# Kernel tuning notes

Hardware: AMD Instinct MI355X
Metric: run time of the kernel (lower is better)

## Reference

```python
import jax, jax.numpy as jnp
import numpy as np

H = 256
V_IN = 32000
V_OUT = 32000
T = 2048


def setup_inputs() -> dict:
    key = jax.random.key(0)
    ks = jax.random.split(key, 16)
    s = 1.0 / np.sqrt(H)
    inp = {
        "src": jax.random.randint(ks[0], (T, 1), 0, V_IN, dtype=jnp.int64 if jax.config.jax_enable_x64 else jnp.int32),
        "trg": jax.random.randint(ks[1], (T, 1), 0, V_OUT, dtype=jnp.int64 if jax.config.jax_enable_x64 else jnp.int32),
        "enc_emb": jax.random.normal(ks[2], (V_IN, H), jnp.float32),
        "enc_W_ih": jax.random.uniform(ks[3], (3 * H, H), jnp.float32, -s, s),
        "enc_W_hh": jax.random.uniform(ks[4], (3 * H, H), jnp.float32, -s, s),
        "enc_b_ih": jax.random.uniform(ks[5], (3 * H,), jnp.float32, -s, s),
        "enc_b_hh": jax.random.uniform(ks[6], (3 * H,), jnp.float32, -s, s),
        "dec_emb": jax.random.normal(ks[7], (V_OUT, H), jnp.float32),
        "dec_W_ih": jax.random.uniform(ks[8], (3 * H, H), jnp.float32, -s, s),
        "dec_W_hh": jax.random.uniform(ks[9], (3 * H, H), jnp.float32, -s, s),
        "dec_b_ih": jax.random.uniform(ks[10], (3 * H,), jnp.float32, -s, s),
        "dec_b_hh": jax.random.uniform(ks[11], (3 * H,), jnp.float32, -s, s),
        "out_W": jax.random.uniform(ks[12], (V_OUT, H), jnp.float32, -s, s),
        "out_b": jax.random.uniform(ks[13], (V_OUT,), jnp.float32, -s, s),
    }
    return inp


def _gru_step(x, h, W_ih, W_hh, b_ih, b_hh):
    # PyTorch GRU cell math. x,h: [H]
    gi = W_ih @ x + b_ih          # [3H]
    gh = W_hh @ h + b_hh          # [3H]
    i_r, i_z, i_n = jnp.split(gi, 3)
    h_r, h_z, h_n = jnp.split(gh, 3)
    r = jax.nn.sigmoid(i_r + h_r)
    z = jax.nn.sigmoid(i_z + h_z)
    n = jnp.tanh(i_n + r * h_n)
    return (1.0 - z) * n + z * h


def reference(src, trg, enc_emb, enc_W_ih, enc_W_hh, enc_b_ih, enc_b_hh,
              dec_emb, dec_W_ih, dec_W_hh, dec_b_ih, dec_b_hh, out_W, out_b):
    src_t = src[:, 0]  # [T], batch forced to 1 by .view(1,1,-1)
    trg_t = trg[:, 0]  # [T]
    h0 = jnp.zeros((H,), enc_emb.dtype)

    def step(h, toks):
        s_tok, t_tok = toks
        # encoder step
        h = _gru_step(enc_emb[s_tok], h, enc_W_ih, enc_W_hh, enc_b_ih, enc_b_hh)
        # decoder step (relu on embedding per source)
        x_d = jax.nn.relu(dec_emb[t_tok])
        h = _gru_step(x_d, h, dec_W_ih, dec_W_hh, dec_b_ih, dec_b_hh)
        logits = out_W @ h + out_b          # [V_OUT]
        return h, jax.nn.log_softmax(logits)

    _, outs = jax.lax.scan(step, h0, (src_t, trg_t))
    return outs[:, None, :]  # [T, 1, V_OUT]
```

## Files before the change

### kernel.cpp

```cpp
#include <hip/hip_runtime.h>
#include <hip/hip_bf16.h>

#define T_STEPS 2048
#define HDIM 256
#define VOUT 32000

#if defined(__has_builtin)
#if __has_builtin(__builtin_amdgcn_sdot4)
#define HAVE_SDOT4 1
#endif
#endif

__device__ __forceinline__ int dot4i8(int a, int b, int c) {
#ifdef HAVE_SDOT4
    return __builtin_amdgcn_sdot4(a, b, c, false);
#else
#pragma unroll
    for (int k = 0; k < 4; ++k) {
        int av = (a << (24 - 8 * k)) >> 24;
        int bv = (b << (24 - 8 * k)) >> 24;
        c += av * bv;
    }
    return c;
#endif
}

__device__ __forceinline__ float fast_sigmoid(float x) {
    return 1.0f / (1.0f + __expf(-x));
}
__device__ __forceinline__ float fast_tanh(float x) {
    float ax = fabsf(x);
    float e = __expf(-2.0f * ax);
    float t = 1.0f - 2.0f * e / (1.0f + e);
    return copysignf(t, x);
}

__global__ void k_quant(const float* __restrict__ W, int* __restrict__ wq,
                        float* __restrict__ sc) {
    int row = blockIdx.x;
    int t = threadIdx.x;
    float4 w = ((const float4*)(W + (size_t)row * HDIM))[t];
    float m = fmaxf(fmaxf(fabsf(w.x), fabsf(w.y)), fmaxf(fabsf(w.z), fabsf(w.w)));
#pragma unroll
    for (int off = 32; off; off >>= 1) m = fmaxf(m, __shfl_xor(m, off));
    float inv = (m > 0.0f) ? 127.0f / m : 0.0f;
    float scale = (m > 0.0f) ? m * (1.0f / 127.0f) : 0.0f;
    int q0 = __float2int_rn(w.x * inv); q0 = max(-127, min(127, q0));
    int q1 = __float2int_rn(w.y * inv); q1 = max(-127, min(127, q1));
    int q2 = __float2int_rn(w.z * inv); q2 = max(-127, min(127, q2));
    int q3 = __float2int_rn(w.w * inv); q3 = max(-127, min(127, q3));
    int packed = (q0 & 255) | ((q1 & 255) << 8) | ((q2 & 255) << 16) | ((q3 & 255) << 24);
    wq[row * 64 + t] = packed;
    if (t == 0) sc[row] = scale;
}

__global__ __launch_bounds__(256) void k_gi(const int* __restrict__ toks,
                                            const float* __restrict__ emb,
                                            const float* __restrict__ W,
                                            const float* __restrict__ b,
                                            float* __restrict__ gi, int do_relu) {
    __shared__ float4 xs[64];
    int t = blockIdx.x;
    int tid = threadIdx.x;
    int tok = toks[t];
    if (tid < 64) {
        float4 x = ((const float4*)(emb + (size_t)tok * HDIM))[tid];
        if (do_relu) {
            x.x = fmaxf(x.x, 0.0f); x.y = fmaxf(x.y, 0.0f);
            x.z = fmaxf(x.z, 0.0f); x.w = fmaxf(x.w, 0.0f);
        }
        xs[tid] = x;
    }
    __syncthreads();
#pragma unroll
    for (int g = 0; g < 3; ++g) {
        int row = tid + g * 256;
        const float4* wr = (const float4*)(W + (size_t)row * HDIM);
        float acc = b[row];
#pragma unroll 16
        for (int k = 0; k < 64; ++k) {
            float4 w = wr[k];
            float4 x = xs[k];
            acc += w.x * x.x + w.y * x.y + w.z * x.z + w.w * x.w;
        }
        gi[(size_t)t * 768 + row] = acc;
    }
}

__global__ __launch_bounds__(768, 3) void k_gru(
    const int* __restrict__ wq_e, const float* __restrict__ sc_e,
    const float* __restrict__ bhh_e, const float* __restrict__ gi_e,
    const int* __restrict__ wq_d, const float* __restrict__ sc_d,
    const float* __restrict__ bhh_d, const float* __restrict__ gi_d,
    float* __restrict__ h_all) {
    __shared__ float Y[768];
    __shared__ float GN[256];
    __shared__ __align__(16) int HQ[64];

    const int tid = threadIdx.x;
    const int row = tid;

    int we[64], wd[64];
    {
        const int4* pe = (const int4*)(wq_e + row * 64);
        const int4* pd = (const int4*)(wq_d + row * 64);
#pragma unroll
        for (int i = 0; i < 16; ++i) {
            int4 a = pe[i];
            int4 bq = pd[i];
            we[4 * i + 0] = a.x;  we[4 * i + 1] = a.y;
            we[4 * i + 2] = a.z;  we[4 * i + 3] = a.w;
            wd[4 * i + 0] = bq.x; wd[4 * i + 1] = bq.y;
            wd[4 * i + 2] = bq.z; wd[4 * i + 3] = bq.w;
        }
    }
    const float se = sc_e[row] * (1.0f / 127.0f);
    const float sd = sc_d[row] * (1.0f / 127.0f);
    const float be = bhh_e[row];
    const float bd = bhh_d[row];
    const bool lead = (tid < 256);
    float h = 0.0f;
    if (tid < 64) HQ[tid] = 0;
    __syncthreads();

    const float* ge = gi_e + row;
    const float* gd = gi_d + row;
    float* hop = h_all + tid;

    for (int t = 0; t < T_STEPS; ++t) {
        float gie = *ge; ge += 768;
        float gid = *gd; gd += 768;

        {
            int acc = 0;
            const int4* hq4 = (const int4*)HQ;
#pragma unroll
            for (int c = 0; c < 16; ++c) {
                int4 hv = hq4[c];
                acc = dot4i8(we[4 * c + 0], hv.x, acc);
                acc = dot4i8(we[4 * c + 1], hv.y, acc);
                acc = dot4i8(we[4 * c + 2], hv.z, acc);
                acc = dot4i8(we[4 * c + 3], hv.w, acc);
            }
            float y = se * (float)acc + be;
            if (row < 512) Y[row] = y + gie;
            else { Y[row] = y; GN[row - 512] = gie; }
        }
        __syncthreads();
        if (lead) {
            float r = fast_sigmoid(Y[tid]);
            float z = fast_sigmoid(Y[256 + tid]);
            float n = fast_tanh(GN[tid] + r * Y[512 + tid]);
            h = (1.0f - z) * n + z * h;
            ((signed char*)HQ)[tid] = (signed char)__float2int_rn(h * 127.0f);
        }
        __syncthreads();

        {
            int acc = 0;
            const int4* hq4 = (const int4*)HQ;
#pragma unroll
            for (int c = 0; c < 16; ++c) {
                int4 hv = hq4[c];
                acc = dot4i8(wd[4 * c + 0], hv.x, acc);
                acc = dot4i8(wd[4 * c + 1], hv.y, acc);
                acc = dot4i8(wd[4 * c + 2], hv.z, acc);
                acc = dot4i8(wd[4 * c + 3], hv.w, acc);
            }
            float y = sd * (float)acc + bd;
            if (row < 512) Y[row] = y + gid;
            else { Y[row] = y; GN[row - 512] = gid; }
        }
        __syncthreads();
        if (lead) {
            float r = fast_sigmoid(Y[tid]);
            float z = fast_sigmoid(Y[256 + tid]);
            float n = fast_tanh(GN[tid] + r * Y[512 + tid]);
            h = (1.0f - z) * n + z * h;
            *hop = h; hop += 256;
            ((signed char*)HQ)[tid] = (signed char)__float2int_rn(h * 127.0f);
        }
        __syncthreads();
    }
}

__global__ __launch_bounds__(256) void k_logits(const float* __restrict__ h_all,
                                                const float* __restrict__ out_W,
                                                const float* __restrict__ out_b,
                                                float* __restrict__ out) {
    __shared__ float As[64][68];
    __shared__ float Bs[64][68];
    const int vb = blockIdx.x * 64;
    const int tb = blockIdx.y * 64;
    const int tid = threadIdx.x;
    const int tx = tid & 15;
    const int ty = tid >> 4;
    const int tl = tid & 63;
    const int kg = tid >> 6;

    float acc[4][4];
#pragma unroll
    for (int i = 0; i < 4; ++i)
#pragma unroll
        for (int j = 0; j < 4; ++j) acc[i][j] = 0.0f;

    for (int k0 = 0; k0 < HDIM; k0 += 64) {
#pragma unroll
        for (int j = 0; j < 4; ++j) {
            float4 a = *(const float4*)&h_all[(size_t)(tb + tl) * HDIM + k0 + kg * 16 + 4 * j];
            int kk = kg * 16 + 4 * j;
            As[kk + 0][tl] = a.x; As[kk + 1][tl] = a.y;
            As[kk + 2][tl] = a.z; As[kk + 3][tl] = a.w;
            float4 b = *(const float4*)&out_W[(size_t)(vb + tl) * HDIM + k0 + kg * 16 + 4 * j];
            Bs[kk + 0][tl] = b.x; Bs[kk + 1][tl] = b.y;
            Bs[kk + 2][tl] = b.z; Bs[kk + 3][tl] = b.w;
        }
        __syncthreads();
#pragma unroll 16
        for (int k = 0; k < 64; ++k) {
            float4 a = *(const float4*)&As[k][ty * 4];
            float4 b = *(const float4*)&Bs[k][tx * 4];
            acc[0][0] += a.x * b.x; acc[0][1] += a.x * b.y; acc[0][2] += a.x * b.z; acc[0][3] += a.x * b.w;
            acc[1][0] += a.y * b.x; acc[1][1] += a.y * b.y; acc[1][2] += a.y * b.z; acc[1][3] += a.y * b.w;
            acc[2][0] += a.z * b.x; acc[2][1] += a.z * b.y; acc[2][2] += a.z * b.z; acc[2][3] += a.z * b.w;
            acc[3][0] += a.w * b.x; acc[3][1] += a.w * b.y; acc[3][2] += a.w * b.z; acc[3][3] += a.w * b.w;
        }
        __syncthreads();
    }
    float4 bias = *(const float4*)&out_b[vb + tx * 4];
#pragma unroll
    for (int i = 0; i < 4; ++i) {
        float4 o;
        o.x = acc[i][0] + bias.x; o.y = acc[i][1] + bias.y;
        o.z = acc[i][2] + bias.z; o.w = acc[i][3] + bias.w;
        *(float4*)&out[(size_t)(tb + ty * 4 + i) * VOUT + vb + tx * 4] = o;
    }
}

__global__ __launch_bounds__(256) void k_lse(const float* __restrict__ out,
                                             float* __restrict__ lse) {
    const int t = blockIdx.x;
    const int tid = threadIdx.x;
    const float* rowp = out + (size_t)t * VOUT;
    float m = -3.0e38f, l = 0.0f;
    for (int v = tid; v < VOUT; v += 256) {
        float x = rowp[v];
        float M = fmaxf(m, x);
        l = l * __expf(m - M) + __expf(x - M);
        m = M;
    }
#pragma unroll
    for (int off = 32; off; off >>= 1) {
        float m2 = __shfl_xor(m, off);
        float l2 = __shfl_xor(l, off);
        float M = fmaxf(m, m2);
        l = l * __expf(m - M) + l2 * __expf(m2 - M);
        m = M;
    }
    __shared__ float sm[4], sl[4];
    int lane = tid & 63, w = tid >> 6;
    if (lane == 0) { sm[w] = m; sl[w] = l; }
    __syncthreads();
    if (tid == 0) {
        float M = fmaxf(fmaxf(sm[0], sm[1]), fmaxf(sm[2], sm[3]));
        float L = sl[0] * __expf(sm[0] - M) + sl[1] * __expf(sm[1] - M) +
                  sl[2] * __expf(sm[2] - M) + sl[3] * __expf(sm[3] - M);
        lse[t] = M + __logf(L);
    }
}

__global__ __launch_bounds__(256) void k_sub(float* __restrict__ out,
                                             const float* __restrict__ lse) {
    const int t = blockIdx.y;
    const int v4 = blockIdx.x * 256 + threadIdx.x;
    if (v4 < VOUT / 4) {
        float s = lse[t];
        float4* p = (float4*)(out + (size_t)t * VOUT) + v4;
        float4 o = *p;
        o.x -= s; o.y -= s; o.z -= s; o.w -= s;
        *p = o;
    }
}

extern "C" void kernel_launch(void* const* d_in, const int* in_sizes, int n_in,
                              void* d_out, int out_size, void* d_ws, size_t ws_size,
                              hipStream_t stream) {
    (void)in_sizes; (void)n_in; (void)out_size; (void)ws_size;
    const int*   src      = (const int*)d_in[0];
    const int*   trg      = (const int*)d_in[1];
    const float* enc_emb  = (const float*)d_in[2];
    const float* enc_W_ih = (const float*)d_in[3];
    const float* enc_W_hh = (const float*)d_in[4];
    const float* enc_b_ih = (const float*)d_in[5];
    const float* enc_b_hh = (const float*)d_in[6];
    const float* dec_emb  = (const float*)d_in[7];
    const float* dec_W_ih = (const float*)d_in[8];
    const float* dec_W_hh = (const float*)d_in[9];
    const float* dec_b_ih = (const float*)d_in[10];
    const float* dec_b_hh = (const float*)d_in[11];
    const float* out_W    = (const float*)d_in[12];
    const float* out_b    = (const float*)d_in[13];
    float* out = (float*)d_out;

    char* ws = (char*)d_ws;
    float* gi_e  = (float*)ws; ws += (size_t)T_STEPS * 768 * 4;
    float* gi_d  = (float*)ws; ws += (size_t)T_STEPS * 768 * 4;
    float* h_all = (float*)ws; ws += (size_t)T_STEPS * HDIM * 4;
    float* lse   = (float*)ws; ws += (size_t)T_STEPS * 4;
    float* sc_e  = (float*)ws; ws += 768 * 4;
    float* sc_d  = (float*)ws; ws += 768 * 4;
    int*   wq_e  = (int*)ws;   ws += 768 * 64 * 4;
    int*   wq_d  = (int*)ws;   ws += 768 * 64 * 4;

    k_quant<<<768, 64, 0, stream>>>(enc_W_hh, wq_e, sc_e);
    k_quant<<<768, 64, 0, stream>>>(dec_W_hh, wq_d, sc_d);
    k_gi<<<T_STEPS, 256, 0, stream>>>(src, enc_emb, enc_W_ih, enc_b_ih, gi_e, 0);
    k_gi<<<T_STEPS, 256, 0, stream>>>(trg, dec_emb, dec_W_ih, dec_b_ih, gi_d, 1);
    k_gru<<<1, 768, 0, stream>>>(wq_e, sc_e, enc_b_hh, gi_e,
                                 wq_d, sc_d, dec_b_hh, gi_d, h_all);
    k_logits<<<dim3(VOUT / 64, T_STEPS / 64), 256, 0, stream>>>(h_all, out_W, out_b, out);
    k_lse<<<T_STEPS, 256, 0, stream>>>(out, lse);
    k_sub<<<dim3(32, T_STEPS), 256, 0, stream>>>(out, lse);
}
```

Baseline: 4.596 ms.

## Use bf16 MFMA for logits GEMM and split GRU row dot products across lanes

The output projection GEMM now runs on bf16 MFMA 16x16x32 instructions instead of an fp32 LDS-tiled FMA loop, with new conversion kernels that turn out_W and h_all into bf16. Separately, the GRU recurrent matvec is reorganised so each lane handles a quarter of the K dimension for four rows, combined with xor shuffles. This shortens the serial dot-product chain on the per-step critical path. Converting to bf16 lowers logits precision, and the extra conversion passes add memory traffic.

Result: faster. 4.463 ms (-2.9%).

```diff
diff --git a/kernel.cpp b/kernel.cpp
--- a/kernel.cpp
+++ b/kernel.cpp
@@ -4,6 +4,9 @@
 #define T_STEPS 2048
 #define HDIM 256
 #define VOUT 32000
+
+typedef short short8 __attribute__((ext_vector_type(8)));
+typedef float f32x4 __attribute__((ext_vector_type(4)));
 
 #if defined(__has_builtin)
 #if __has_builtin(__builtin_amdgcn_sdot4)
@@ -52,6 +55,22 @@
     int packed = (q0 & 255) | ((q1 & 255) << 8) | ((q2 & 255) << 16) | ((q3 & 255) << 24);
     wq[row * 64 + t] = packed;
     if (t == 0) sc[row] = scale;
+}
+
+__global__ __launch_bounds__(256) void k_cvt(const float* __restrict__ in,
+                                             unsigned short* __restrict__ out, int n4) {
+    int i = blockIdx.x * 256 + threadIdx.x;
+    if (i < n4) {
+        float4 v = ((const float4*)in)[i];
+        unsigned int u[4] = {__float_as_uint(v.x), __float_as_uint(v.y),
+                             __float_as_uint(v.z), __float_as_uint(v.w)};
+        ushort4 o;
+        o.x = (unsigned short)((u[0] + 0x7FFFu + ((u[0] >> 16) & 1)) >> 16);
+        o.y = (unsigned short)((u[1] + 0x7FFFu + ((u[1] >> 16) & 1)) >> 16);
+        o.z = (unsigned short)((u[2] + 0x7FFFu + ((u[2] >> 16) & 1)) >> 16);
+        o.w = (unsigned short)((u[3] + 0x7FFFu + ((u[3] >> 16) & 1)) >> 16);
+        ((ushort4*)out)[i] = o;
+    }
 }
 
 __global__ __launch_bounds__(256) void k_gi(const int* __restrict__ toks,
@@ -98,53 +117,74 @@
     __shared__ __align__(16) int HQ[64];
 
     const int tid = threadIdx.x;
-    const int row = tid;
-
-    int we[64], wd[64];
-    {
-        const int4* pe = (const int4*)(wq_e + row * 64);
-        const int4* pd = (const int4*)(wq_d + row * 64);
-#pragma unroll
-        for (int i = 0; i < 16; ++i) {
+    const int w = tid >> 6;
+    const int l = tid & 63;
+    const int c = l & 3;
+    const int g = l >> 2;
+
+    int we[4][16], wd[4][16];
+#pragma unroll
+    for (int j = 0; j < 4; ++j) {
+        const int4* pe = (const int4*)(wq_e + ((w * 64 + g * 4 + j) * 64 + c * 16));
+        const int4* pd = (const int4*)(wq_d + ((w * 64 + g * 4 + j) * 64 + c * 16));
+#pragma unroll
+        for (int i = 0; i < 4; ++i) {
             int4 a = pe[i];
+            we[j][4 * i + 0] = a.x; we[j][4 * i + 1] = a.y;
+            we[j][4 * i + 2] = a.z; we[j][4 * i + 3] = a.w;
             int4 bq = pd[i];
-            we[4 * i + 0] = a.x;  we[4 * i + 1] = a.y;
-            we[4 * i + 2] = a.z;  we[4 * i + 3] = a.w;
-            wd[4 * i + 0] = bq.x; wd[4 * i + 1] = bq.y;
-            wd[4 * i + 2] = bq.z; wd[4 * i + 3] = bq.w;
-        }
-    }
-    const float se = sc_e[row] * (1.0f / 127.0f);
-    const float sd = sc_d[row] * (1.0f / 127.0f);
-    const float be = bhh_e[row];
-    const float bd = bhh_d[row];
+            wd[j][4 * i + 0] = bq.x; wd[j][4 * i + 1] = bq.y;
+            wd[j][4 * i + 2] = bq.z; wd[j][4 * i + 3] = bq.w;
+        }
+    }
+    const float se = sc_e[tid] * (1.0f / 127.0f);
+    const float sd = sc_d[tid] * (1.0f / 127.0f);
+    const float be = bhh_e[tid];
+    const float bd = bhh_d[tid];
     const bool lead = (tid < 256);
+    const int c0 = c & 1;
+    const int c1 = c & 2;
     float h = 0.0f;
     if (tid < 64) HQ[tid] = 0;
     __syncthreads();
 
-    const float* ge = gi_e + row;
-    const float* gd = gi_d + row;
+    const float* ge = gi_e + tid;
+    const float* gd = gi_d + tid;
     float* hop = h_all + tid;
+    const int4* hq4 = (const int4*)HQ;
 
     for (int t = 0; t < T_STEPS; ++t) {
         float gie = *ge; ge += 768;
         float gid = *gd; gd += 768;
 
         {
-            int acc = 0;
-            const int4* hq4 = (const int4*)HQ;
-#pragma unroll
-            for (int c = 0; c < 16; ++c) {
-                int4 hv = hq4[c];
-                acc = dot4i8(we[4 * c + 0], hv.x, acc);
-                acc = dot4i8(we[4 * c + 1], hv.y, acc);
-                acc = dot4i8(we[4 * c + 2], hv.z, acc);
-                acc = dot4i8(we[4 * c + 3], hv.w, acc);
+            int4 h0 = hq4[c * 4 + 0];
+            int4 h1 = hq4[c * 4 + 1];
+            int4 h2 = hq4[c * 4 + 2];
+            int4 h3 = hq4[c * 4 + 3];
+            int p[4];
+#pragma unroll
+            for (int j = 0; j < 4; ++j) {
+                int a = 0;
+                a = dot4i8(we[j][0], h0.x, a);  a = dot4i8(we[j][1], h0.y, a);
+                a = dot4i8(we[j][2], h0.z, a);  a = dot4i8(we[j][3], h0.w, a);
+                a = dot4i8(we[j][4], h1.x, a);  a = dot4i8(we[j][5], h1.y, a);
+                a = dot4i8(we[j][6], h1.z, a);  a = dot4i8(we[j][7], h1.w, a);
+                a = dot4i8(we[j][8], h2.x, a);  a = dot4i8(we[j][9], h2.y, a);
+                a = dot4i8(we[j][10], h2.z, a); a = dot4i8(we[j][11], h2.w, a);
+                a = dot4i8(we[j][12], h3.x, a); a = dot4i8(we[j][13], h3.y, a);
+                a = dot4i8(we[j][14], h3.z, a); a = dot4i8(we[j][15], h3.w, a);
+                p[j] = a;
             }
-            float y = se * (float)acc + be;
-            if (row < 512) Y[row] = y + gie;
-            else { Y[row] = y; GN[row - 512] = gie; }
+            int s0 = c0 ? p[0] : p[1];
+            int s1 = c0 ? p[2] : p[3];
+            int r0 = (c0 ? p[1] : p[0]) + __shfl_xor(s0, 1);
+            int r1 = (c0 ? p[3] : p[2]) + __shfl_xor(s1, 1);
+            int s2 = c1 ? r0 : r1;
+            int fin = (c1 ? r1 : r0) + __shfl_xor(s2, 2);
+            float y = se * (float)fin + be;
+            if (tid < 512) Y[tid] = y + gie;
+            else { Y[tid] = y; GN[tid - 512] = gie; }
         }
         __syncthreads();
         if (lead) {
@@ -157,19 +197,33 @@
         __syncthreads();
 
         {
-            int acc = 0;
-            const int4* hq4 = (const int4*)HQ;
-#pragma unroll
-            for (int c = 0; c < 16; ++c) {
-                int4 hv = hq4[c];
-                acc = dot4i8(wd[4 * c + 0], hv.x, acc);
-                acc = dot4i8(wd[4 * c + 1], hv.y, acc);
-                acc = dot4i8(wd[4 * c + 2], hv.z, acc);
-                acc = dot4i8(wd[4 * c + 3], hv.w, acc);
+            int4 h0 = hq4[c * 4 + 0];
+            int4 h1 = hq4[c * 4 + 1];
+            int4 h2 = hq4[c * 4 + 2];
+            int4 h3 = hq4[c * 4 + 3];
+            int p[4];
+#pragma unroll
+            for (int j = 0; j < 4; ++j) {
+                int a = 0;
+                a = dot4i8(wd[j][0], h0.x, a);  a = dot4i8(wd[j][1], h0.y, a);
+                a = dot4i8(wd[j][2], h0.z, a);  a = dot4i8(wd[j][3], h0.w, a);
+                a = dot4i8(wd[j][4], h1.x, a);  a = dot4i8(wd[j][5], h1.y, a);
+                a = dot4i8(wd[j][6], h1.z, a);  a = dot4i8(wd[j][7], h1.w, a);
+                a = dot4i8(wd[j][8], h2.x, a);  a = dot4i8(wd[j][9], h2.y, a);
+                a = dot4i8(wd[j][10], h2.z, a); a = dot4i8(wd[j][11], h2.w, a);
+                a = dot4i8(wd[j][12], h3.x, a); a = dot4i8(wd[j][13], h3.y, a);
+                a = dot4i8(wd[j][14], h3.z, a); a = dot4i8(wd[j][15], h3.w, a);
+                p[j] = a;
             }
-            float y = sd * (float)acc + bd;
-            if (row < 512) Y[row] = y + gid;
-            else { Y[row] = y; GN[row - 512] = gid; }
+            int s0 = c0 ? p[0] : p[1];
+            int s1 = c0 ? p[2] : p[3];
+            int r0 = (c0 ? p[1] : p[0]) + __shfl_xor(s0, 1);
+            int r1 = (c0 ? p[3] : p[2]) + __shfl_xor(s1, 1);
+            int s2 = c1 ? r0 : r1;
+            int fin = (c1 ? r1 : r0) + __shfl_xor(s2, 2);
+            float y = sd * (float)fin + bd;
+            if (tid < 512) Y[tid] = y + gid;
+            else { Y[tid] = y; GN[tid - 512] = gid; }
         }
         __syncthreads();
         if (lead) {
@@ -184,56 +238,47 @@
     }
 }
 
-__global__ __launch_bounds__(256) void k_logits(const float* __restrict__ h_all,
-                                                const float* __restrict__ out_W,
+__global__ __launch_bounds__(256) void k_logits(const unsigned short* __restrict__ hb,
+                                                const unsigned short* __restrict__ wb,
                                                 const float* __restrict__ out_b,
                                                 float* __restrict__ out) {
-    __shared__ float As[64][68];
-    __shared__ float Bs[64][68];
     const int vb = blockIdx.x * 64;
     const int tb = blockIdx.y * 64;
-    const int tid = threadIdx.x;
-    const int tx = tid & 15;
-    const int ty = tid >> 4;
-    const int tl = tid & 63;
-    const int kg = tid >> 6;
-
-    float acc[4][4];
-#pragma unroll
-    for (int i = 0; i < 4; ++i)
-#pragma unroll
-        for (int j = 0; j < 4; ++j) acc[i][j] = 0.0f;
-
-    for (int k0 = 0; k0 < HDIM; k0 += 64) {
-#pragma unroll
-        for (int j = 0; j < 4; ++j) {
-            float4 a = *(const float4*)&h_all[(size_t)(tb + tl) * HDIM + k0 + kg * 16 + 4 * j];
-            int kk = kg * 16 + 4 * j;
-            As[kk + 0][tl] = a.x; As[kk + 1][tl] = a.y;
-            As[kk + 2][tl] = a.z; As[kk + 3][tl] = a.w;
-            float4 b = *(const float4*)&out_W[(size_t)(vb + tl) * HDIM + k0 + kg * 16 + 4 * j];
-            Bs[kk + 0][tl] = b.x; Bs[kk + 1][tl] = b.y;
-            Bs[kk + 2][tl] = b.z; Bs[kk + 3][tl] = b.w;
-        }
-        __syncthreads();
-#pragma unroll 16
-        for (int k = 0; k < 64; ++k) {
-            float4 a = *(const float4*)&As[k][ty * 4];
-            float4 b = *(const float4*)&Bs[k][tx * 4];
-            acc[0][0] += a.x * b.x; acc[0][1] += a.x * b.y; acc[0][2] += a.x * b.z; acc[0][3] += a.x * b.w;
-            acc[1][0] += a.y * b.x; acc[1][1] += a.y * b.y; acc[1][2] += a.y * b.z; acc[1][3] += a.y * b.w;
-            acc[2][0] += a.z * b.x; acc[2][1] += a.z * b.y; acc[2][2] += a.z * b.z; acc[2][3] += a.z * b.w;
-            acc[3][0] += a.w * b.x; acc[3][1] += a.w * b.y; acc[3][2] += a.w * b.z; acc[3][3] += a.w * b.w;
-        }
-        __syncthreads();
-    }
-    float4 bias = *(const float4*)&out_b[vb + tx * 4];
-#pragma unroll
-    for (int i = 0; i < 4; ++i) {
-        float4 o;
-        o.x = acc[i][0] + bias.x; o.y = acc[i][1] + bias.y;
-        o.z = acc[i][2] + bias.z; o.w = acc[i][3] + bias.w;
-        *(float4*)&out[(size_t)(tb + ty * 4 + i) * VOUT + vb + tx * 4] = o;
+    const int w = threadIdx.x >> 6;
+    const int l = threadIdx.x & 63;
+    const int m = l & 15;
+    const int q = l >> 4;
+
+    const unsigned short* aptr = hb + (size_t)(tb + w * 16 + m) * HDIM + q * 8;
+    const unsigned short* bptr = wb + (size_t)(vb + m) * HDIM + q * 8;
+
+    short8 af[8];
+#pragma unroll
+    for (int kt = 0; kt < 8; ++kt) af[kt] = *(const short8*)(aptr + kt * 32);
+
+    f32x4 acc[4];
+#pragma unroll
+    for (int nt = 0; nt < 4; ++nt)
+#pragma unroll
+        for (int r = 0; r < 4; ++r) acc[nt][r] = 0.0f;
+
+#pragma unroll
+    for (int nt = 0; nt < 4; ++nt) {
+        const unsigned short* bp = bptr + (size_t)nt * 16 * HDIM;
+#pragma unroll
+        for (int kt = 0; kt < 8; ++kt) {
+            short8 bf = *(const short8*)(bp + kt * 32);
+            acc[nt] = __builtin_amdgcn_mfma_f32_16x16x32_bf16(af[kt], bf, acc[nt], 0, 0, 0);
+        }
+    }
+#pragma unroll
+    for (int nt = 0; nt < 4; ++nt) {
+        float bias = out_b[vb + nt * 16 + m];
+#pragma unroll
+        for (int r = 0; r < 4; ++r) {
+            out[(size_t)(tb + w * 16 + q * 4 + r) * VOUT + vb + nt * 16 + m] =
+                acc[nt][r] + bias;
+        }
     }
 }
 
@@ -258,8 +303,8 @@
         m = M;
     }
     __shared__ float sm[4], sl[4];
-    int lane = tid & 63, w = tid >> 6;
-    if (lane == 0) { sm[w] = m; sl[w] = l; }
+    int lane = tid & 63, wv = tid >> 6;
+    if (lane == 0) { sm[wv] = m; sl[wv] = l; }
     __syncthreads();
     if (tid == 0) {
         float M = fmaxf(fmaxf(sm[0], sm[1]), fmaxf(sm[2], sm[3]));
@@ -311,14 +356,18 @@
     float* sc_d  = (float*)ws; ws += 768 * 4;
     int*   wq_e  = (int*)ws;   ws += 768 * 64 * 4;
     int*   wq_d  = (int*)ws;   ws += 768 * 64 * 4;
+    unsigned short* h_bf = (unsigned short*)ws; ws += (size_t)T_STEPS * HDIM * 2;
+    unsigned short* w_bf = (unsigned short*)ws; ws += (size_t)VOUT * HDIM * 2;
 
     k_quant<<<768, 64, 0, stream>>>(enc_W_hh, wq_e, sc_e);
     k_quant<<<768, 64, 0, stream>>>(dec_W_hh, wq_d, sc_d);
+    k_cvt<<<(VOUT * HDIM / 4 + 255) / 256, 256, 0, stream>>>(out_W, w_bf, VOUT * HDIM / 4);
     k_gi<<<T_STEPS, 256, 0, stream>>>(src, enc_emb, enc_W_ih, enc_b_ih, gi_e, 0);
     k_gi<<<T_STEPS, 256, 0, stream>>>(trg, dec_emb, dec_W_ih, dec_b_ih, gi_d, 1);
     k_gru<<<1, 768, 0, stream>>>(wq_e, sc_e, enc_b_hh, gi_e,
                                  wq_d, sc_d, dec_b_hh, gi_d, h_all);
-    k_logits<<<dim3(VOUT / 64, T_STEPS / 64), 256, 0, stream>>>(h_all, out_W, out_b, out);
+    k_cvt<<<(T_STEPS * HDIM / 4 + 255) / 256, 256, 0, stream>>>(h_all, h_bf, T_STEPS * HDIM / 4);
+    k_logits<<<dim3(VOUT / 64, T_STEPS / 64), 256, 0, stream>>>(h_bf, w_bf, out_b, out);
     k_lse<<<T_STEPS, 256, 0, stream>>>(out, lse);
     k_sub<<<dim3(32, T_STEPS), 256, 0, stream>>>(out, lse);
 }
```
